# Performance work log

Hardware: AMD Instinct MI355X
Metric: run time of the kernel (lower is better)

Reference implementation:

```python
import jax, jax.numpy as jnp
import numpy as np

N = 100000      # nodes
F_IN = 512      # input features
HID = 256       # hidden
C = 50          # classes
E = 1_600_000   # edges
K = 10          # APPNP iterations
ALPHA = 1.0     # teleport prob (as hard-coded in source: APPNP(10, 1))


def setup_inputs() -> dict:
    key = jax.random.key(0)
    k1, k2, k3, k4, k5, k6 = jax.random.split(key, 6)
    x = jax.random.normal(k1, (N, F_IN), dtype=jnp.float32)
    edge_index = jax.random.randint(k2, (2, E), 0, N, dtype=jnp.int32)
    # Linear params (torch nn.Linear default init scale ~ 1/sqrt(fan_in))
    W1 = jax.random.uniform(k3, (F_IN, HID), jnp.float32, -1.0, 1.0) / np.sqrt(F_IN)
    b1 = jax.random.uniform(k4, (HID,), jnp.float32, -1.0, 1.0) / np.sqrt(F_IN)
    W2 = jax.random.uniform(k5, (HID, C), jnp.float32, -1.0, 1.0) / np.sqrt(HID)
    b2 = jax.random.uniform(k6, (C,), jnp.float32, -1.0, 1.0) / np.sqrt(HID)
    return {"x": x, "edge_index": edge_index, "W1": W1, "b1": b1, "W2": W2, "b2": b2}


def _appnp(h, edge_index):
    # gcn_norm with self-loops: A_hat = D^{-1/2} (A + I) D^{-1/2}
    loops = jnp.arange(N, dtype=edge_index.dtype)
    src = jnp.concatenate([edge_index[0], loops])  # message sources
    dst = jnp.concatenate([edge_index[1], loops])  # aggregation targets
    deg = jax.ops.segment_sum(jnp.ones_like(dst, dtype=h.dtype), dst, num_segments=N)
    dinv = jnp.where(deg > 0, jax.lax.rsqrt(deg), 0.0)
    norm = (dinv[src] * dinv[dst])[:, None]  # [E+N, 1]

    def step(z, _):
        agg = jax.ops.segment_sum(norm * z[src], dst, num_segments=N)  # [N, C]
        z = (1.0 - ALPHA) * agg + ALPHA * h
        return z, None

    z, _ = jax.lax.scan(step, h, None, length=K)
    return z


def reference(x, edge_index, W1, b1, W2, b2):
    # eval mode: dropout is identity
    h = jax.nn.relu(x @ W1 + b1)   # [N, HID]
    h = h @ W2 + b2                # [N, C]
    z = _appnp(h, edge_index)      # K-step personalized-pagerank propagation
    return jax.nn.log_softmax(z, axis=1)
```

## Files before the change

### kernel.cpp

```cpp
#include <hip/hip_runtime.h>
#include <cstdint>
#include <cstddef>

#define NROWS 100000
#define FIN 512
#define HIDDEN 256
#define NCLS 50

typedef __attribute__((ext_vector_type(8))) short s16x8;
typedef __attribute__((ext_vector_type(4))) float f32x4;

__device__ __forceinline__ unsigned short f2bf(float f) {
  unsigned int u = __float_as_uint(f);
  u += 0x7fffu + ((u >> 16) & 1u);
  return (unsigned short)(u >> 16);
}

__device__ __forceinline__ unsigned int cvt_pk_bf16(float lo, float hi) {
  unsigned int r;
  asm("v_cvt_pk_bf16_f32 %0, %1, %2" : "=v"(r) : "v"(lo), "v"(hi));
  return r;
}

__device__ __forceinline__ void gload_lds16(const void* g, void* l) {
  __builtin_amdgcn_global_load_lds(
      (const __attribute__((address_space(1))) void*)g,
      (__attribute__((address_space(3))) void*)l, 16, 0, 0);
}

__device__ __forceinline__ f32x4 mfma_bf16(s16x8 a, s16x8 b, f32x4 c) {
  return __builtin_amdgcn_mfma_f32_16x16x32_bf16(a, b, c, 0, 0, 0);
}

__global__ __launch_bounds__(256) void prep_kernel(
    const float* __restrict__ W1, const float* __restrict__ W2,
    unsigned short* __restrict__ w1t, unsigned short* __restrict__ w2t) {
  __shared__ float tile[64][65];
  const int b = blockIdx.x, t = threadIdx.x;
  if (b < 32) {
    const int k0 = (b >> 2) * 64, n0 = (b & 3) * 64;
    const int rq = t >> 6, col = t & 63;
#pragma unroll
    for (int i = 0; i < 16; ++i) {
      int row = i * 4 + rq;
      tile[row][col] = W1[(size_t)(k0 + row) * HIDDEN + n0 + col];
    }
    __syncthreads();
#pragma unroll
    for (int i = 0; i < 16; ++i) {
      int n = i * 4 + rq;
      w1t[(size_t)(n0 + n) * FIN + k0 + col] = f2bf(tile[col][n]);
    }
  } else {
    const int b2i = b - 32;
#pragma unroll
    for (int i = 0; i < 16; ++i) {
      int idx = t + i * 256;
      int c = idx >> 6;
      int k = b2i * 64 + (idx & 63);
      float v = (c < NCLS) ? W2[(size_t)k * NCLS + c] : 0.0f;
      w2t[(size_t)c * HIDDEN + k] = f2bf(v);
    }
  }
}

__global__ __launch_bounds__(512, 4) void fused_kernel(
    const float* __restrict__ x, const unsigned short* __restrict__ w1t,
    const unsigned short* __restrict__ w2t, const float* __restrict__ b1,
    const float* __restrict__ b2, float* __restrict__ out) {
  __shared__ char smem[65536];
  float* const Abase = (float*)smem;
  unsigned short* const Bbase = (unsigned short*)(smem + 32768);

  const int t = threadIdx.x;
  const int lane = t & 63, wid = t >> 6;
  const int q = lane & 15, half = lane >> 4;
  const int wr = wid >> 1, wc = wid & 1;
  const int bm = blockIdx.x;

  auto stage_A = [&](float* buf, int k0) {
#pragma unroll
    for (int i = 0; i < 2; ++i) {
      int c = t + i * 512;
      int row = c >> 3, s = c & 7;
      int grow = bm * 128 + row;
      if (grow > NROWS - 1) grow = NROWS - 1;
      gload_lds16(x + (size_t)grow * FIN + k0 + ((s ^ (row & 7)) << 2),
                  buf + c * 4);
    }
  };
  auto stage_B = [&](unsigned short* buf, int k0) {
#pragma unroll
    for (int i = 0; i < 2; ++i) {
      int c = t + i * 512;
      int col = c >> 2, s = c & 3;
      gload_lds16(w1t + (size_t)col * FIN + k0 + ((s ^ ((col >> 1) & 3)) << 3),
                  buf + c * 8);
    }
  };

  f32x4 acc[8][2];
  const f32x4 z4 = {0.f, 0.f, 0.f, 0.f};
#pragma unroll
  for (int i = 0; i < 8; ++i)
#pragma unroll
    for (int j = 0; j < 2; ++j) acc[i][j] = z4;

  stage_A(Abase, 0);
  stage_B(Bbase, 0);
  __syncthreads();

  for (int ks = 0; ks < 16; ++ks) {
    const int cur = ks & 1;
    float* Ac = Abase + cur * 4096;
    unsigned short* Bc = Bbase + cur * 8192;
    if (ks < 15) {
      stage_A(Abase + (cur ^ 1) * 4096, (ks + 1) * 32);
      stage_B(Bbase + (cur ^ 1) * 8192, (ks + 1) * 32);
    }

    s16x8 af[2];
#pragma unroll
    for (int m = 0; m < 2; ++m) {
      const int row = wr * 32 + m * 16 + q;
      const int cb = row * 8;
      f32x4 lo = *(const f32x4*)(Ac + (cb + ((half * 2) ^ (q & 7))) * 4);
      f32x4 hi = *(const f32x4*)(Ac + (cb + ((half * 2 + 1) ^ (q & 7))) * 4);
      union { unsigned int u[4]; s16x8 v; } cvu;
      cvu.u[0] = cvt_pk_bf16(lo[0], lo[1]);
      cvu.u[1] = cvt_pk_bf16(lo[2], lo[3]);
      cvu.u[2] = cvt_pk_bf16(hi[0], hi[1]);
      cvu.u[3] = cvt_pk_bf16(hi[2], hi[3]);
      af[m] = cvu.v;
    }

#pragma unroll
    for (int n = 0; n < 8; ++n) {
      const int col = wc * 128 + n * 16 + q;
      s16x8 bf = *(const s16x8*)(Bc + col * 32 + ((half ^ ((q >> 1) & 3)) << 3));
      acc[n][0] = mfma_bf16(bf, af[0], acc[n][0]);
      acc[n][1] = mfma_bf16(bf, af[1], acc[n][1]);
    }
    __syncthreads();
  }

  unsigned short* const hls = (unsigned short*)smem;
  unsigned short* const wls = Bbase;
  const int p_of_wave = wid >> 2;

#pragma unroll
  for (int i = 0; i < 4; ++i) {
    int c = t + i * 512;
    int row = c >> 5, s = c & 31;
    gload_lds16(w2t + (size_t)row * HIDDEN + ((s ^ (row & 7)) << 3), wls + c * 8);
  }

  auto write_h = [&]() {
#pragma unroll
    for (int i = 0; i < 8; ++i) {
      const int hc0 = wc * 128 + i * 16 + half * 4;
      const float4 b4 = *(const float4*)(b1 + hc0);
      const int ch = hc0 >> 3;
#pragma unroll
      for (int j = 0; j < 2; ++j) {
        const int rl = (wr & 1) * 32 + j * 16 + q;
        const float v0 = fmaxf(acc[i][j][0] + b4.x, 0.0f);
        const float v1 = fmaxf(acc[i][j][1] + b4.y, 0.0f);
        const float v2 = fmaxf(acc[i][j][2] + b4.z, 0.0f);
        const float v3 = fmaxf(acc[i][j][3] + b4.w, 0.0f);
        uint2 u;
        u.x = cvt_pk_bf16(v0, v1);
        u.y = cvt_pk_bf16(v2, v3);
        const int slot = (ch + rl) & 31;
        *(uint2*)(hls + rl * 256 + slot * 8 + (half & 1) * 4) = u;
      }
    }
  };

  auto gemm2_pass = [&](int p) {
    f32x4 acc2[4];
#pragma unroll
    for (int n = 0; n < 4; ++n) acc2[n] = z4;
    const int arl = (wid & 3) * 16 + q;
#pragma unroll
    for (int ks = 0; ks < HIDDEN; ks += 32) {
      const int g = (ks >> 3) + half;
      s16x8 a2 = *(const s16x8*)(hls + arl * 256 + (((g + arl) & 31) << 3));
#pragma unroll
      for (int n = 0; n < 4; ++n) {
        const int c = n * 16 + q;
        s16x8 b2f = *(const s16x8*)(wls + c * 256 + ((g ^ (c & 7)) << 3));
        acc2[n] = mfma_bf16(a2, b2f, acc2[n]);
      }
    }
    float bias2[4];
#pragma unroll
    for (int n = 0; n < 4; ++n) {
      const int c = n * 16 + q;
      bias2[n] = (c < NCLS) ? b2[c] : 0.0f;
    }
#pragma unroll
    for (int r = 0; r < 4; ++r) {
      float vals[4];
      float mx = -1e30f;
#pragma unroll
      for (int n = 0; n < 4; ++n) {
        const int c = n * 16 + q;
        float v = acc2[n][r] + bias2[n];
        vals[n] = v;
        if (c < NCLS) mx = fmaxf(mx, v);
      }
      for (int off = 8; off >= 1; off >>= 1)
        mx = fmaxf(mx, __shfl_xor(mx, off, 64));
      float s = 0.f;
#pragma unroll
      for (int n = 0; n < 4; ++n) {
        const int c = n * 16 + q;
        if (c < NCLS) s += __expf(vals[n] - mx);
      }
      for (int off = 8; off >= 1; off >>= 1) s += __shfl_xor(s, off, 64);
      const float lz = __logf(s);
      const int rowg = bm * 128 + p * 64 + (wid & 3) * 16 + half * 4 + r;
      if (rowg < NROWS) {
#pragma unroll
        for (int n = 0; n < 4; ++n) {
          const int c = n * 16 + q;
          if (c < NCLS) out[(size_t)rowg * NCLS + c] = vals[n] - mx - lz;
        }
      }
    }
  };

  if (p_of_wave == 0) write_h();
  __syncthreads();
  if (p_of_wave == 0) gemm2_pass(0);
  __syncthreads();
  if (p_of_wave == 1) write_h();
  __syncthreads();
  if (p_of_wave == 1) gemm2_pass(1);
}

extern "C" void kernel_launch(void* const* d_in, const int* in_sizes, int n_in,
                              void* d_out, int out_size, void* d_ws, size_t ws_size,
                              hipStream_t stream) {
  const float* x  = (const float*)d_in[0];
  const float* W1 = (const float*)d_in[2];
  const float* b1 = (const float*)d_in[3];
  const float* W2 = (const float*)d_in[4];
  const float* b2 = (const float*)d_in[5];
  float* out = (float*)d_out;

  char* ws = (char*)d_ws;
  unsigned short* w1t = (unsigned short*)(ws);
  unsigned short* w2t = (unsigned short*)(ws + 262144);

  prep_kernel<<<36, 256, 0, stream>>>(W1, W2, w1t, w2t);
  fused_kernel<<<(NROWS + 127) / 128, 512, 0, stream>>>(x, w1t, w2t, b1, b2, out);
}
```

Baseline: 64.84 us.

## Load A directly to registers, 4-deep B ring, single-pass GEMM2 epilogue

The x tile now goes straight from global memory into registers, two k-steps ahead, instead of being staged through LDS. W1 tiles flow through a 4-slot LDS ring with a prefetch distance of 2, so each k-step needs one raw s_barrier instead of two __syncthreads. The epilogue writes both 64-row halves of h to separate LDS regions at once and runs GEMM2 in one pass, reading W2 directly from global/L1 rather than staging it. This removes LDS traffic and barriers for A and halves the epilogue phases, at the cost of more registers and uncoalesced 32-byte per-lane global loads for A.

```diff
diff --git a/kernel.cpp b/kernel.cpp
--- a/kernel.cpp
+++ b/kernel.cpp
@@ -69,8 +69,7 @@
     const unsigned short* __restrict__ w2t, const float* __restrict__ b1,
     const float* __restrict__ b2, float* __restrict__ out) {
   __shared__ char smem[65536];
-  float* const Abase = (float*)smem;
-  unsigned short* const Bbase = (unsigned short*)(smem + 32768);
+  unsigned short* const Bring = (unsigned short*)smem;
 
   const int t = threadIdx.x;
   const int lane = t & 63, wid = t >> 6;
@@ -78,24 +77,37 @@
   const int wr = wid >> 1, wc = wid & 1;
   const int bm = blockIdx.x;
 
-  auto stage_A = [&](float* buf, int k0) {
-#pragma unroll
-    for (int i = 0; i < 2; ++i) {
-      int c = t + i * 512;
-      int row = c >> 3, s = c & 7;
-      int grow = bm * 128 + row;
-      if (grow > NROWS - 1) grow = NROWS - 1;
-      gload_lds16(x + (size_t)grow * FIN + k0 + ((s ^ (row & 7)) << 2),
-                  buf + c * 4);
-    }
+  const float* aptr[2];
+#pragma unroll
+  for (int m = 0; m < 2; ++m) {
+    int r = bm * 128 + wr * 32 + m * 16 + q;
+    if (r > NROWS - 1) r = NROWS - 1;
+    aptr[m] = x + (size_t)r * FIN + half * 8;
+  }
+
+  const unsigned short* bsrc[2];
+  int bdst[2];
+#pragma unroll
+  for (int i = 0; i < 2; ++i) {
+    const int c = t + i * 512;
+    const int col = c >> 2, s = c & 3;
+    bsrc[i] = w1t + (size_t)col * FIN + ((s ^ ((col >> 1) & 3)) << 3);
+    bdst[i] = c * 8;
+  }
+
+  auto stage_B = [&](int rg, int kstep) {
+#pragma unroll
+    for (int i = 0; i < 2; ++i)
+      gload_lds16(bsrc[i] + kstep * 32, Bring + rg * 8192 + bdst[i]);
   };
-  auto stage_B = [&](unsigned short* buf, int k0) {
-#pragma unroll
-    for (int i = 0; i < 2; ++i) {
-      int c = t + i * 512;
-      int col = c >> 2, s = c & 3;
-      gload_lds16(w1t + (size_t)col * FIN + k0 + ((s ^ ((col >> 1) & 3)) << 3),
-                  buf + c * 8);
+
+  float4 ra[2][2][2];
+  auto load_A = [&](int sl, int kstep) {
+#pragma unroll
+    for (int m = 0; m < 2; ++m) {
+      const float* p = aptr[m] + kstep * 32;
+      ra[sl][m][0] = ((const float4*)p)[0];
+      ra[sl][m][1] = ((const float4*)p)[1];
     }
   };
 
@@ -106,34 +118,34 @@
 #pragma unroll
     for (int j = 0; j < 2; ++j) acc[i][j] = z4;
 
-  stage_A(Abase, 0);
-  stage_B(Bbase, 0);
-  __syncthreads();
-
-  for (int ks = 0; ks < 16; ++ks) {
-    const int cur = ks & 1;
-    float* Ac = Abase + cur * 4096;
-    unsigned short* Bc = Bbase + cur * 8192;
-    if (ks < 15) {
-      stage_A(Abase + (cur ^ 1) * 4096, (ks + 1) * 32);
-      stage_B(Bbase + (cur ^ 1) * 8192, (ks + 1) * 32);
-    }
+  stage_B(0, 0);
+  stage_B(1, 1);
+  load_A(0, 0);
+  load_A(1, 1);
+
+#pragma unroll
+  for (int k = 0; k < 16; ++k) {
+    const int sl = k & 1, rg = k & 3;
+    if (k + 2 < 16) stage_B((k + 2) & 3, k + 2);
 
     s16x8 af[2];
 #pragma unroll
     for (int m = 0; m < 2; ++m) {
-      const int row = wr * 32 + m * 16 + q;
-      const int cb = row * 8;
-      f32x4 lo = *(const f32x4*)(Ac + (cb + ((half * 2) ^ (q & 7))) * 4);
-      f32x4 hi = *(const f32x4*)(Ac + (cb + ((half * 2 + 1) ^ (q & 7))) * 4);
+      const float4 lo = ra[sl][m][0], hi = ra[sl][m][1];
       union { unsigned int u[4]; s16x8 v; } cvu;
-      cvu.u[0] = cvt_pk_bf16(lo[0], lo[1]);
-      cvu.u[1] = cvt_pk_bf16(lo[2], lo[3]);
-      cvu.u[2] = cvt_pk_bf16(hi[0], hi[1]);
-      cvu.u[3] = cvt_pk_bf16(hi[2], hi[3]);
+      cvu.u[0] = cvt_pk_bf16(lo.x, lo.y);
+      cvu.u[1] = cvt_pk_bf16(lo.z, lo.w);
+      cvu.u[2] = cvt_pk_bf16(hi.x, hi.y);
+      cvu.u[3] = cvt_pk_bf16(hi.z, hi.w);
       af[m] = cvu.v;
     }
-
+    if (k + 2 < 16) load_A(sl, k + 2);
+
+    __builtin_amdgcn_sched_barrier(0);
+    __builtin_amdgcn_s_barrier();
+    __builtin_amdgcn_sched_barrier(0);
+
+    const unsigned short* Bc = Bring + rg * 8192;
 #pragma unroll
     for (int n = 0; n < 8; ++n) {
       const int col = wc * 128 + n * 16 + q;
@@ -141,103 +153,85 @@
       acc[n][0] = mfma_bf16(bf, af[0], acc[n][0]);
       acc[n][1] = mfma_bf16(bf, af[1], acc[n][1]);
     }
-    __syncthreads();
-  }
-
-  unsigned short* const hls = (unsigned short*)smem;
-  unsigned short* const wls = Bbase;
-  const int p_of_wave = wid >> 2;
-
-#pragma unroll
-  for (int i = 0; i < 4; ++i) {
-    int c = t + i * 512;
-    int row = c >> 5, s = c & 31;
-    gload_lds16(w2t + (size_t)row * HIDDEN + ((s ^ (row & 7)) << 3), wls + c * 8);
-  }
-
-  auto write_h = [&]() {
-#pragma unroll
-    for (int i = 0; i < 8; ++i) {
-      const int hc0 = wc * 128 + i * 16 + half * 4;
-      const float4 b4 = *(const float4*)(b1 + hc0);
-      const int ch = hc0 >> 3;
-#pragma unroll
-      for (int j = 0; j < 2; ++j) {
-        const int rl = (wr & 1) * 32 + j * 16 + q;
-        const float v0 = fmaxf(acc[i][j][0] + b4.x, 0.0f);
-        const float v1 = fmaxf(acc[i][j][1] + b4.y, 0.0f);
-        const float v2 = fmaxf(acc[i][j][2] + b4.z, 0.0f);
-        const float v3 = fmaxf(acc[i][j][3] + b4.w, 0.0f);
-        uint2 u;
-        u.x = cvt_pk_bf16(v0, v1);
-        u.y = cvt_pk_bf16(v2, v3);
-        const int slot = (ch + rl) & 31;
-        *(uint2*)(hls + rl * 256 + slot * 8 + (half & 1) * 4) = u;
-      }
-    }
-  };
-
-  auto gemm2_pass = [&](int p) {
-    f32x4 acc2[4];
-#pragma unroll
-    for (int n = 0; n < 4; ++n) acc2[n] = z4;
-    const int arl = (wid & 3) * 16 + q;
-#pragma unroll
-    for (int ks = 0; ks < HIDDEN; ks += 32) {
-      const int g = (ks >> 3) + half;
-      s16x8 a2 = *(const s16x8*)(hls + arl * 256 + (((g + arl) & 31) << 3));
+  }
+  __syncthreads();
+
+  unsigned short* const hls = (unsigned short*)(smem + (wr >> 1) * 32768);
+#pragma unroll
+  for (int i = 0; i < 8; ++i) {
+    const int hc0 = wc * 128 + i * 16 + half * 4;
+    const float4 b4 = *(const float4*)(b1 + hc0);
+    const int ch = hc0 >> 3;
+#pragma unroll
+    for (int j = 0; j < 2; ++j) {
+      const int rl = (wr & 1) * 32 + j * 16 + q;
+      const float v0 = fmaxf(acc[i][j][0] + b4.x, 0.0f);
+      const float v1 = fmaxf(acc[i][j][1] + b4.y, 0.0f);
+      const float v2 = fmaxf(acc[i][j][2] + b4.z, 0.0f);
+      const float v3 = fmaxf(acc[i][j][3] + b4.w, 0.0f);
+      uint2 u;
+      u.x = cvt_pk_bf16(v0, v1);
+      u.y = cvt_pk_bf16(v2, v3);
+      const int slot = (ch + rl) & 31;
+      *(uint2*)(hls + rl * 256 + slot * 8 + (half & 1) * 4) = u;
+    }
+  }
+  __syncthreads();
+
+  const int p = wid >> 2, aw = wid & 3;
+  const unsigned short* const hrd = (const unsigned short*)(smem + p * 32768);
+  f32x4 acc2[4];
+#pragma unroll
+  for (int n = 0; n < 4; ++n) acc2[n] = z4;
+  const int arl = aw * 16 + q;
+#pragma unroll
+  for (int j = 0; j < 8; ++j) {
+    const int g = j * 4 + half;
+    s16x8 a2 = *(const s16x8*)(hrd + arl * 256 + (((g + arl) & 31) << 3));
+#pragma unroll
+    for (int n = 0; n < 4; ++n) {
+      const int c = n * 16 + q;
+      s16x8 b2f = *(const s16x8*)(w2t + (size_t)c * HIDDEN + j * 32 + half * 8);
+      acc2[n] = mfma_bf16(a2, b2f, acc2[n]);
+    }
+  }
+
+  float bias2[4];
+#pragma unroll
+  for (int n = 0; n < 4; ++n) {
+    const int c = n * 16 + q;
+    bias2[n] = (c < NCLS) ? b2[c] : 0.0f;
+  }
+#pragma unroll
+  for (int r = 0; r < 4; ++r) {
+    float vals[4];
+    float mx = -1e30f;
+#pragma unroll
+    for (int n = 0; n < 4; ++n) {
+      const int c = n * 16 + q;
+      float v = acc2[n][r] + bias2[n];
+      vals[n] = v;
+      if (c < NCLS) mx = fmaxf(mx, v);
+    }
+    for (int off = 8; off >= 1; off >>= 1)
+      mx = fmaxf(mx, __shfl_xor(mx, off, 64));
+    float s = 0.f;
+#pragma unroll
+    for (int n = 0; n < 4; ++n) {
+      const int c = n * 16 + q;
+      if (c < NCLS) s += __expf(vals[n] - mx);
+    }
+    for (int off = 8; off >= 1; off >>= 1) s += __shfl_xor(s, off, 64);
+    const float lz = __logf(s);
+    const int rowg = bm * 128 + p * 64 + aw * 16 + half * 4 + r;
+    if (rowg < NROWS) {
 #pragma unroll
       for (int n = 0; n < 4; ++n) {
         const int c = n * 16 + q;
-        s16x8 b2f = *(const s16x8*)(wls + c * 256 + ((g ^ (c & 7)) << 3));
-        acc2[n] = mfma_bf16(a2, b2f, acc2[n]);
+        if (c < NCLS) out[(size_t)rowg * NCLS + c] = vals[n] - mx - lz;
       }
     }
-    float bias2[4];
-#pragma unroll
-    for (int n = 0; n < 4; ++n) {
-      const int c = n * 16 + q;
-      bias2[n] = (c < NCLS) ? b2[c] : 0.0f;
-    }
-#pragma unroll
-    for (int r = 0; r < 4; ++r) {
-      float vals[4];
-      float mx = -1e30f;
-#pragma unroll
-      for (int n = 0; n < 4; ++n) {
-        const int c = n * 16 + q;
-        float v = acc2[n][r] + bias2[n];
-        vals[n] = v;
-        if (c < NCLS) mx = fmaxf(mx, v);
-      }
-      for (int off = 8; off >= 1; off >>= 1)
-        mx = fmaxf(mx, __shfl_xor(mx, off, 64));
-      float s = 0.f;
-#pragma unroll
-      for (int n = 0; n < 4; ++n) {
-        const int c = n * 16 + q;
-        if (c < NCLS) s += __expf(vals[n] - mx);
-      }
-      for (int off = 8; off >= 1; off >>= 1) s += __shfl_xor(s, off, 64);
-      const float lz = __logf(s);
-      const int rowg = bm * 128 + p * 64 + (wid & 3) * 16 + half * 4 + r;
-      if (rowg < NROWS) {
-#pragma unroll
-        for (int n = 0; n < 4; ++n) {
-          const int c = n * 16 + q;
-          if (c < NCLS) out[(size_t)rowg * NCLS + c] = vals[n] - mx - lz;
-        }
-      }
-    }
-  };
-
-  if (p_of_wave == 0) write_h();
-  __syncthreads();
-  if (p_of_wave == 0) gemm2_pass(0);
-  __syncthreads();
-  if (p_of_wave == 1) write_h();
-  __syncthreads();
-  if (p_of_wave == 1) gemm2_pass(1);
+  }
 }
 
 extern "C" void kernel_launch(void* const* d_in, const int* in_sizes, int n_in,
```

After: 165.9 us. 156% more time.
